# Kernel tuning notes

Hardware: AMD Instinct MI355X
Metric: run time of the kernel (lower is better)

The kernel has to match this reference:

```python
import jax, jax.numpy as jnp
import numpy as np

B, S, H = 4, 4096, 2048
NH, HD = 16, 128
DFF = 8192
CAPACITY = 0.5
EPS = 1e-5


def setup_inputs() -> dict:
    key = jax.random.key(0)
    ks = jax.random.split(key, 11)
    s_h = 1.0 / np.sqrt(H)
    s_f = 1.0 / np.sqrt(DFF)
    return {
        "hidden_states": jax.random.normal(ks[0], (B, S, H), jnp.float32),
        "w_router": jax.random.normal(ks[1], (H,), jnp.float32) * s_h,
        "b_router": jnp.zeros((1,), jnp.float32),
        "Wq": jax.random.normal(ks[2], (H, H), jnp.float32) * s_h,
        "Wk": jax.random.normal(ks[3], (H, H), jnp.float32) * s_h,
        "Wv": jax.random.normal(ks[4], (H, H), jnp.float32) * s_h,
        "Wo": jax.random.normal(ks[5], (H, H), jnp.float32) * s_h,
        "w_gate": jax.random.normal(ks[6], (H, DFF), jnp.float32) * s_h,
        "w_up": jax.random.normal(ks[7], (H, DFF), jnp.float32) * s_h,
        "w_down": jax.random.normal(ks[8], (DFF, H), jnp.float32) * s_f,
        "norm1_w": jnp.ones((H,), jnp.float32),
        "norm2_w": jnp.ones((H,), jnp.float32),
    }


def _rmsnorm(x, w):
    var = jnp.mean(jnp.square(x), axis=-1, keepdims=True)
    return x * jax.lax.rsqrt(var + EPS) * w


def reference(hidden_states, w_router, b_router, Wq, Wk, Wv, Wo,
              w_gate, w_up, w_down, norm1_w, norm2_w):
    x = hidden_states  # [B,S,H]
    # --- router: sigmoid(Wx+b), select top-k per row, ties via >= threshold ---
    logits = jnp.einsum("bsh,h->bs", x, w_router) + b_router[0]
    weights = jax.nn.sigmoid(logits)  # [B,S]
    k = max(1, int(CAPACITY * S))
    topk_vals, _ = jax.lax.top_k(weights, k)
    threshold = topk_vals[:, -1:]
    mask = weights >= threshold  # [B,S] bool

    # --- full block, computed per-token (attention is over seq_len==1) ---
    n1 = _rmsnorm(x, norm1_w)
    q = (n1 @ Wq).reshape(B, S, NH, HD)
    kk = (n1 @ Wk).reshape(B, S, NH, HD)
    v = (n1 @ Wv).reshape(B, S, NH, HD)
    # each selected token is its own length-1 sequence -> softmax over 1 pos == 1
    scores = jnp.einsum("bshd,bshd->bsh", q, kk) / np.sqrt(HD)
    attn_w = jax.nn.softmax(scores[..., None], axis=-1)  # [B,S,NH,1], all ones
    ctx = (attn_w * v).reshape(B, S, H)
    attn_out = ctx @ Wo

    res = x + attn_out
    n2 = _rmsnorm(res, norm2_w)
    ffn = (jax.nn.silu(n2 @ w_gate) * (n2 @ w_up)) @ w_down
    out_full = res + ffn

    # scatter back: non-selected tokens pass through unchanged
    out = jnp.where(mask[..., None], out_full, x)
    return out
```

## Files before the change

### kernel.cpp

```cpp
#include <hip/hip_runtime.h>
#include <cstdint>
#include <cstddef>

#define B_    4
#define S_    4096
#define H_    2048
#define DFF_  8192
#define KSEL  2048
#define CAP   2304
#define NTILE_PB 18
#define TCAP  (B_*CAP)
#define NRT   (TCAP/128)

typedef unsigned short ushort_t;
typedef __attribute__((ext_vector_type(8))) __bf16 bf16x8;
typedef __attribute__((ext_vector_type(4))) float f32x4;

__device__ __forceinline__ ushort_t f2bf(float f) {
  union { float f; uint32_t u; } v; v.f = f;
  uint32_t u = v.u;
  return (ushort_t)((u + 0x7FFFu + ((u >> 16) & 1u)) >> 16);
}

__device__ __forceinline__ void gload16(const void* g, void* l) {
  __builtin_amdgcn_global_load_lds(
      (const __attribute__((address_space(1))) void*)g,
      (__attribute__((address_space(3))) void*)l, 16, 0, 0);
}

__global__ __launch_bounds__(256) void wconvT_k(const float* __restrict__ W,
                                                ushort_t* __restrict__ Wt,
                                                int K, int N) {
  __shared__ float tile[64][65];
  int k0 = blockIdx.x * 64, n0 = blockIdx.y * 64;
  int tx = threadIdx.x & 63, ty = threadIdx.x >> 6;
  #pragma unroll
  for (int yy = ty; yy < 64; yy += 4)
    tile[yy][tx] = W[(size_t)(k0 + yy) * N + n0 + tx];
  __syncthreads();
  #pragma unroll
  for (int yy = ty; yy < 64; yy += 4)
    Wt[(size_t)(n0 + yy) * K + k0 + tx] = f2bf(tile[tx][yy]);
}

__global__ __launch_bounds__(256) void router_k(const float* __restrict__ x,
                                                const float* __restrict__ wr,
                                                const float* __restrict__ br,
                                                float* __restrict__ wts) {
  int t = blockIdx.x * 4 + (threadIdx.x >> 6);
  int lane = threadIdx.x & 63;
  const float4* xr = (const float4*)(x + (size_t)t * H_);
  const float4* w4 = (const float4*)wr;
  float s = 0.f;
  #pragma unroll
  for (int j = 0; j < 8; ++j) {
    float4 a = xr[lane + 64 * j], b = w4[lane + 64 * j];
    s = fmaf(a.x, b.x, s); s = fmaf(a.y, b.y, s);
    s = fmaf(a.z, b.z, s); s = fmaf(a.w, b.w, s);
  }
  #pragma unroll
  for (int o = 32; o > 0; o >>= 1) s += __shfl_xor(s, o, 64);
  if (lane == 0) wts[t] = 1.f / (1.f + expf(-(s + br[0])));
}

__global__ __launch_bounds__(1024) void kth_k(const float* __restrict__ wts,
                                              float* __restrict__ thr) {
  __shared__ float a[S_];
  int b = blockIdx.x, tid = threadIdx.x;
  const float* wb = wts + b * S_;
  for (int i = tid; i < S_; i += 1024) a[i] = wb[i];
  for (int size = 2; size <= S_; size <<= 1) {
    for (int stride = size >> 1; stride > 0; stride >>= 1) {
      __syncthreads();
      for (int t = tid; t < S_ / 2; t += 1024) {
        int i = ((t / stride) * (stride << 1)) + (t % stride);
        int j = i + stride;
        bool up = ((i & size) == 0);
        float ai = a[i], aj = a[j];
        if ((ai > aj) == up) { a[i] = aj; a[j] = ai; }
      }
    }
  }
  __syncthreads();
  if (tid == 0) thr[b] = a[S_ - KSEL];
}

__global__ __launch_bounds__(1024) void compact_k(const float* __restrict__ wts,
                                                  const float* __restrict__ thr,
                                                  int* __restrict__ idx,
                                                  int* __restrict__ counts) {
  __shared__ int sc[1024];
  int b = blockIdx.x, tid = threadIdx.x;
  float th = thr[b];
  int m[4], cnt = 0;
  #pragma unroll
  for (int e = 0; e < 4; ++e) {
    m[e] = (wts[b * S_ + tid * 4 + e] >= th) ? 1 : 0;
    cnt += m[e];
  }
  sc[tid] = cnt;
  __syncthreads();
  for (int off = 1; off < 1024; off <<= 1) {
    int add = (tid >= off) ? sc[tid - off] : 0;
    __syncthreads();
    sc[tid] += add;
    __syncthreads();
  }
  int excl = sc[tid] - cnt;
  int total = sc[1023];
  int cl = total < CAP ? total : CAP;
  #pragma unroll
  for (int e = 0; e < 4; ++e) {
    if (m[e]) {
      if (excl < CAP) idx[b * CAP + excl] = b * S_ + tid * 4 + e;
      excl++;
    }
  }
  for (int j2 = tid; j2 < CAP; j2 += 1024)
    if (j2 >= cl) idx[b * CAP + j2] = -1;
  if (tid == 0) counts[b] = cl;
}

template <int MODE>
__global__ __launch_bounds__(256) void rms_k(const float* __restrict__ src,
                                             const float* __restrict__ w,
                                             const int* __restrict__ idx,
                                             const int* __restrict__ counts,
                                             ushort_t* __restrict__ dst) {
  int r = blockIdx.x * 4 + (threadIdx.x >> 6);
  int lane = threadIdx.x & 63;
  ushort4* drow = (ushort4*)(dst + (size_t)r * H_);
  const float* s;
  if (MODE == 0) {
    int b = r / CAP, local = r % CAP;
    if (local >= counts[b]) {
      ushort4 z; z.x = z.y = z.z = z.w = 0;
      #pragma unroll
      for (int j = 0; j < 8; ++j) drow[lane + 64 * j] = z;
      return;
    }
    s = src + (size_t)idx[r] * H_;
  } else {
    s = src + (size_t)r * H_;
  }
  const float4* s4 = (const float4*)s;
  float4 v[8];
  float ss = 0.f;
  #pragma unroll
  for (int j = 0; j < 8; ++j) {
    v[j] = s4[lane + 64 * j];
    ss = fmaf(v[j].x, v[j].x, ss); ss = fmaf(v[j].y, v[j].y, ss);
    ss = fmaf(v[j].z, v[j].z, ss); ss = fmaf(v[j].w, v[j].w, ss);
  }
  #pragma unroll
  for (int o = 32; o > 0; o >>= 1) ss += __shfl_xor(ss, o, 64);
  float rstd = rsqrtf(ss * (1.f / H_) + 1e-5f);
  const float4* w4 = (const float4*)w;
  #pragma unroll
  for (int j = 0; j < 8; ++j) {
    float4 ww = w4[lane + 64 * j];
    ushort4 o4;
    o4.x = f2bf(v[j].x * rstd * ww.x);
    o4.y = f2bf(v[j].y * rstd * ww.y);
    o4.z = f2bf(v[j].z * rstd * ww.z);
    o4.w = f2bf(v[j].w * rstd * ww.w);
    drow[lane + 64 * j] = o4;
  }
}

__global__ void copy_k(const float4* __restrict__ in, float4* __restrict__ out,
                       int n) {
  int i = blockIdx.x * blockDim.x + threadIdx.x;
  int stride = gridDim.x * blockDim.x;
  for (; i < n; i += stride) out[i] = in[i];
}

template <int EPI>
__global__ __launch_bounds__(256) void gemm_k(const ushort_t* __restrict__ A,
                                              const ushort_t* __restrict__ Bt,
                                              int K, int N,
                                              const int* __restrict__ counts,
                                              const int* __restrict__ idx,
                                              const float* __restrict__ xres,
                                              float* __restrict__ outf,
                                              ushort_t* __restrict__ outh) {
  const int nt = N >> 7;
  const int rt = (int)blockIdx.x / nt;
  const int ct = (int)blockIdx.x % nt;
  const int bb = rt / NTILE_PB;
  const int local0 = (rt % NTILE_PB) << 7;
  if (local0 >= counts[bb]) return;

  __shared__ __align__(16) char lds[32768];
  char* ldsA = lds;
  char* ldsB = lds + 16384;

  const int tid = threadIdx.x;
  const int lane = tid & 63;
  const int wave = tid >> 6;
  const int wm = wave >> 1, wn = wave & 1;

  const int srow = tid >> 3;
  const int c16l = (tid & 7) ^ (srow & 7);
  const size_t Kb = (size_t)K * 2;
  const char* aSrc = (const char*)A + (size_t)(rt * 128 + srow) * Kb + (size_t)c16l * 16;
  const char* bSrc = (const char*)Bt + (size_t)(ct * 128 + srow) * Kb + (size_t)c16l * 16;
  char* aDst = ldsA + wave * 1024;
  char* bDst = ldsB + wave * 1024;

  const int frow = lane & 15;
  const int fk = lane >> 4;
  const int ax = frow & 7;

  f32x4 acc[4][4];
  #pragma unroll
  for (int i = 0; i < 4; ++i)
    #pragma unroll
    for (int j = 0; j < 4; ++j) acc[i][j] = (f32x4){0.f, 0.f, 0.f, 0.f};

  const int nkt = K >> 6;
  for (int kt = 0; kt < nkt; ++kt) {
    __syncthreads();
    #pragma unroll
    for (int inst = 0; inst < 4; ++inst) {
      gload16(aSrc + (size_t)inst * 32 * Kb + (size_t)kt * 128, aDst + inst * 4096);
      gload16(bSrc + (size_t)inst * 32 * Kb + (size_t)kt * 128, bDst + inst * 4096);
    }
    __syncthreads();
    #pragma unroll
    for (int ks = 0; ks < 2; ++ks) {
      bf16x8 af[4], bfv[4];
      #pragma unroll
      for (int i = 0; i < 4; ++i) {
        int ar = wm * 64 + i * 16 + frow;
        af[i] = *(const bf16x8*)(ldsA + ar * 128 + (((ks * 4 + fk) ^ ax) << 4));
        int br2 = wn * 64 + i * 16 + frow;
        bfv[i] = *(const bf16x8*)(ldsB + br2 * 128 + (((ks * 4 + fk) ^ ax) << 4));
      }
      #pragma unroll
      for (int i = 0; i < 4; ++i)
        #pragma unroll
        for (int j = 0; j < 4; ++j)
          acc[i][j] = __builtin_amdgcn_mfma_f32_16x16x32_bf16(af[i], bfv[j],
                                                              acc[i][j], 0, 0, 0);
    }
  }

  const int erow0 = rt * 128 + wm * 64;
  const int ecol0 = ct * 128 + wn * 64;
  const int rq = (lane >> 4) << 2;
  const int cc = lane & 15;
  #pragma unroll
  for (int i = 0; i < 4; ++i) {
    #pragma unroll
    for (int q = 0; q < 4; ++q) {
      int r = erow0 + i * 16 + rq + q;
      if (EPI == 0) {
        #pragma unroll
        for (int j = 0; j < 4; ++j)
          outh[(size_t)r * N + ecol0 + j * 16 + cc] = f2bf(acc[i][j][q]);
      } else if (EPI == 1) {
        int t = idx[r];
        #pragma unroll
        for (int j = 0; j < 4; ++j) {
          int c = ecol0 + j * 16 + cc;
          float xv = (t >= 0) ? xres[(size_t)t * H_ + c] : 0.f;
          outf[(size_t)r * H_ + c] = xv + acc[i][j][q];
        }
      } else {
        int t = idx[r];
        if (t >= 0) {
          #pragma unroll
          for (int j = 0; j < 4; ++j) {
            int c = ecol0 + j * 16 + cc;
            outf[(size_t)t * H_ + c] = xres[(size_t)r * H_ + c] + acc[i][j][q];
          }
        }
      }
    }
  }
}

__global__ __launch_bounds__(256) void gemm_dual_k(const ushort_t* __restrict__ A,
                                                   const ushort_t* __restrict__ Bg,
                                                   const ushort_t* __restrict__ Bu,
                                                   const int* __restrict__ counts,
                                                   ushort_t* __restrict__ Hb) {
  const int nt = DFF_ >> 7;
  const int rt = (int)blockIdx.x / nt;
  const int ct = (int)blockIdx.x % nt;
  const int bb = rt / NTILE_PB;
  const int local0 = (rt % NTILE_PB) << 7;
  if (local0 >= counts[bb]) return;

  __shared__ __align__(16) char lds[49152];
  char* ldsA = lds;
  char* ldsG = lds + 16384;
  char* ldsU = lds + 32768;

  const int tid = threadIdx.x;
  const int lane = tid & 63;
  const int wave = tid >> 6;
  const int wm = wave >> 1, wn = wave & 1;

  const int srow = tid >> 3;
  const int c16l = (tid & 7) ^ (srow & 7);
  const size_t Kb = (size_t)H_ * 2;
  const char* aSrc = (const char*)A + (size_t)(rt * 128 + srow) * Kb + (size_t)c16l * 16;
  const char* gSrc = (const char*)Bg + (size_t)(ct * 128 + srow) * Kb + (size_t)c16l * 16;
  const char* uSrc = (const char*)Bu + (size_t)(ct * 128 + srow) * Kb + (size_t)c16l * 16;
  char* aDst = ldsA + wave * 1024;
  char* gDst = ldsG + wave * 1024;
  char* uDst = ldsU + wave * 1024;

  const int frow = lane & 15;
  const int fk = lane >> 4;
  const int ax = frow & 7;

  f32x4 ag[4][4], au[4][4];
  #pragma unroll
  for (int i = 0; i < 4; ++i)
    #pragma unroll
    for (int j = 0; j < 4; ++j) {
      ag[i][j] = (f32x4){0.f, 0.f, 0.f, 0.f};
      au[i][j] = (f32x4){0.f, 0.f, 0.f, 0.f};
    }

  const int nkt = H_ >> 6;
  for (int kt = 0; kt < nkt; ++kt) {
    __syncthreads();
    #pragma unroll
    for (int inst = 0; inst < 4; ++inst) {
      gload16(aSrc + (size_t)inst * 32 * Kb + (size_t)kt * 128, aDst + inst * 4096);
      gload16(gSrc + (size_t)inst * 32 * Kb + (size_t)kt * 128, gDst + inst * 4096);
      gload16(uSrc + (size_t)inst * 32 * Kb + (size_t)kt * 128, uDst + inst * 4096);
    }
    __syncthreads();
    #pragma unroll
    for (int ks = 0; ks < 2; ++ks) {
      bf16x8 af[4], bg[4], bu[4];
      #pragma unroll
      for (int i = 0; i < 4; ++i) {
        int ar = wm * 64 + i * 16 + frow;
        int br2 = wn * 64 + i * 16 + frow;
        int co = (((ks * 4 + fk) ^ ax) << 4);
        af[i] = *(const bf16x8*)(ldsA + ar * 128 + co);
        bg[i] = *(const bf16x8*)(ldsG + br2 * 128 + co);
        bu[i] = *(const bf16x8*)(ldsU + br2 * 128 + co);
      }
      #pragma unroll
      for (int i = 0; i < 4; ++i)
        #pragma unroll
        for (int j = 0; j < 4; ++j) {
          ag[i][j] = __builtin_amdgcn_mfma_f32_16x16x32_bf16(af[i], bg[j], ag[i][j], 0, 0, 0);
          au[i][j] = __builtin_amdgcn_mfma_f32_16x16x32_bf16(af[i], bu[j], au[i][j], 0, 0, 0);
        }
    }
  }

  const int erow0 = rt * 128 + wm * 64;
  const int ecol0 = ct * 128 + wn * 64;
  const int rq = (lane >> 4) << 2;
  const int cc = lane & 15;
  #pragma unroll
  for (int i = 0; i < 4; ++i)
    #pragma unroll
    for (int q = 0; q < 4; ++q) {
      int r = erow0 + i * 16 + rq + q;
      #pragma unroll
      for (int j = 0; j < 4; ++j) {
        float g = ag[i][j][q], u = au[i][j][q];
        float h = (g / (1.f + expf(-g))) * u;
        Hb[(size_t)r * DFF_ + ecol0 + j * 16 + cc] = f2bf(h);
      }
    }
}

extern "C" void kernel_launch(void* const* d_in, const int* in_sizes, int n_in,
                              void* d_out, int out_size, void* d_ws, size_t ws_size,
                              hipStream_t stream) {
  const float* x   = (const float*)d_in[0];
  const float* wr  = (const float*)d_in[1];
  const float* br  = (const float*)d_in[2];
  const float* Wv  = (const float*)d_in[5];
  const float* Wo  = (const float*)d_in[6];
  const float* Wg  = (const float*)d_in[7];
  const float* Wu  = (const float*)d_in[8];
  const float* Wd  = (const float*)d_in[9];
  const float* n1w = (const float*)d_in[10];
  const float* n2w = (const float*)d_in[11];
  float* out = (float*)d_out;

  char* p = (char*)d_ws;
  auto alloc = [&](size_t bytes) {
    char* r = p;
    p += (bytes + 255) & ~(size_t)255;
    return r;
  };
  ushort_t* WvT = (ushort_t*)alloc((size_t)H_ * H_ * 2);
  ushort_t* WoT = (ushort_t*)alloc((size_t)H_ * H_ * 2);
  ushort_t* WgT = (ushort_t*)alloc((size_t)DFF_ * H_ * 2);
  ushort_t* WuT = (ushort_t*)alloc((size_t)DFF_ * H_ * 2);
  ushort_t* WdT = (ushort_t*)alloc((size_t)H_ * DFF_ * 2);
  float* wts    = (float*)alloc((size_t)B_ * S_ * 4);
  float* thr    = (float*)alloc(256);
  int* counts   = (int*)alloc(256);
  int* idx      = (int*)alloc((size_t)TCAP * 4);
  ushort_t* Xn1 = (ushort_t*)alloc((size_t)TCAP * H_ * 2);
  ushort_t* Vc  = (ushort_t*)alloc((size_t)TCAP * H_ * 2);
  float* RES    = (float*)alloc((size_t)TCAP * H_ * 4);
  ushort_t* Hb  = (ushort_t*)alloc((size_t)TCAP * DFF_ * 2);
  (void)ws_size; (void)in_sizes; (void)n_in; (void)out_size;

  wconvT_k<<<dim3(H_ / 64, H_ / 64), 256, 0, stream>>>(Wv, WvT, H_, H_);
  wconvT_k<<<dim3(H_ / 64, H_ / 64), 256, 0, stream>>>(Wo, WoT, H_, H_);
  wconvT_k<<<dim3(H_ / 64, DFF_ / 64), 256, 0, stream>>>(Wg, WgT, H_, DFF_);
  wconvT_k<<<dim3(H_ / 64, DFF_ / 64), 256, 0, stream>>>(Wu, WuT, H_, DFF_);
  wconvT_k<<<dim3(DFF_ / 64, H_ / 64), 256, 0, stream>>>(Wd, WdT, DFF_, H_);

  router_k<<<(B_ * S_) / 4, 256, 0, stream>>>(x, wr, br, wts);
  kth_k<<<B_, 1024, 0, stream>>>(wts, thr);
  compact_k<<<B_, 1024, 0, stream>>>(wts, thr, idx, counts);

  rms_k<0><<<TCAP / 4, 256, 0, stream>>>(x, n1w, idx, counts, Xn1);

  copy_k<<<2048, 256, 0, stream>>>((const float4*)x, (float4*)out,
                                   (B_ * S_ * H_) / 4);

  gemm_k<0><<<NRT * (H_ / 128), 256, 0, stream>>>(Xn1, WvT, H_, H_, counts, idx,
                                                  nullptr, nullptr, Vc);
  gemm_k<1><<<NRT * (H_ / 128), 256, 0, stream>>>(Vc, WoT, H_, H_, counts, idx,
                                                  x, RES, nullptr);
  rms_k<1><<<TCAP / 4, 256, 0, stream>>>(RES, n2w, idx, counts, Xn1);

  gemm_dual_k<<<NRT * (DFF_ / 128), 256, 0, stream>>>(Xn1, WgT, WuT, counts, Hb);

  gemm_k<2><<<NRT * (H_ / 128), 256, 0, stream>>>(Hb, WdT, DFF_, H_, counts, idx,
                                                  RES, out, nullptr);
}
```

Before: 2.126 ms.

## Replace GEMMs with 256x256 double-buffered 8-wave kernel and split gate/up

Replaces the 128x128 single-buffered GEMM kernels with one 256x256-tile, 512-thread kernel. It uses 128KB of dynamic LDS with double buffering so global-to-LDS prefetch of the next K tile overlaps the MFMA work, and it remaps block IDs in an XCD-aware way. The fused gate/up dual GEMM is split into two passes: the first writes the gate result as bf16, and the second reads it back to apply SiLU times up. This aims for more reuse per tile and hidden load latency, at the cost of extra traffic for the gate intermediate and coarser padding granularity for the per-batch token tiles.

```diff
diff --git a/kernel.cpp b/kernel.cpp
--- a/kernel.cpp
+++ b/kernel.cpp
@@ -8,9 +8,9 @@
 #define DFF_  8192
 #define KSEL  2048
 #define CAP   2304
-#define NTILE_PB 18
+#define TPB   9
 #define TCAP  (B_*CAP)
-#define NRT   (TCAP/128)
+#define NRT   (TCAP/256)
 
 typedef unsigned short ushort_t;
 typedef __attribute__((ext_vector_type(8))) __bf16 bf16x8;
@@ -21,12 +21,23 @@
   uint32_t u = v.u;
   return (ushort_t)((u + 0x7FFFu + ((u >> 16) & 1u)) >> 16);
 }
+__device__ __forceinline__ float bf2f(ushort_t h) {
+  union { uint32_t u; float f; } v; v.u = ((uint32_t)h) << 16;
+  return v.f;
+}
 
 __device__ __forceinline__ void gload16(const void* g, void* l) {
   __builtin_amdgcn_global_load_lds(
       (const __attribute__((address_space(1))) void*)g,
       (__attribute__((address_space(3))) void*)l, 16, 0, 0);
 }
+
+#define SBAR()                                  \
+  do {                                          \
+    asm volatile("" ::: "memory");              \
+    __builtin_amdgcn_s_barrier();               \
+    asm volatile("" ::: "memory");              \
+  } while (0)
 
 __global__ __launch_bounds__(256) void wconvT_k(const float* __restrict__ W,
                                                 ushort_t* __restrict__ Wt,
@@ -176,204 +187,158 @@
 }
 
 template <int EPI>
-__global__ __launch_bounds__(256) void gemm_k(const ushort_t* __restrict__ A,
-                                              const ushort_t* __restrict__ Bt,
-                                              int K, int N,
-                                              const int* __restrict__ counts,
-                                              const int* __restrict__ idx,
-                                              const float* __restrict__ xres,
-                                              float* __restrict__ outf,
-                                              ushort_t* __restrict__ outh) {
-  const int nt = N >> 7;
-  const int rt = (int)blockIdx.x / nt;
-  const int ct = (int)blockIdx.x % nt;
-  const int bb = rt / NTILE_PB;
-  const int local0 = (rt % NTILE_PB) << 7;
+__global__ __launch_bounds__(512, 2) void gemm8_k(
+    const ushort_t* __restrict__ A,
+    const ushort_t* __restrict__ Bt,
+    int K, int N, int nct,
+    const int* __restrict__ counts,
+    const int* __restrict__ idx,
+    const float* __restrict__ xres,
+    const ushort_t* __restrict__ gsrc,
+    float* __restrict__ outf,
+    ushort_t* __restrict__ outh) {
+  const int nwg = (int)gridDim.x;
+  const int bid = (int)blockIdx.x;
+  const int cpx = nwg >> 3;
+  const int wg = (bid & 7) * cpx + (bid >> 3);
+  const int rt = wg / nct;
+  const int ct = wg % nct;
+  const int bb = rt / TPB;
+  const int local0 = (rt % TPB) << 8;
   if (local0 >= counts[bb]) return;
 
-  __shared__ __align__(16) char lds[32768];
-  char* ldsA = lds;
-  char* ldsB = lds + 16384;
-
-  const int tid = threadIdx.x;
+  extern __shared__ __align__(16) char lds[];
+
+  const int tid = (int)threadIdx.x;
   const int lane = tid & 63;
   const int wave = tid >> 6;
-  const int wm = wave >> 1, wn = wave & 1;
+  const int wm = wave >> 2;
+  const int wn = wave & 3;
 
   const int srow = tid >> 3;
-  const int c16l = (tid & 7) ^ (srow & 7);
+  const int schunk = (tid & 7) ^ (srow & 7);
   const size_t Kb = (size_t)K * 2;
-  const char* aSrc = (const char*)A + (size_t)(rt * 128 + srow) * Kb + (size_t)c16l * 16;
-  const char* bSrc = (const char*)Bt + (size_t)(ct * 128 + srow) * Kb + (size_t)c16l * 16;
-  char* aDst = ldsA + wave * 1024;
-  char* bDst = ldsB + wave * 1024;
+  const char* aS = (const char*)A + (size_t)(rt * 256 + srow) * Kb + (size_t)schunk * 16;
+  const char* bS = (const char*)Bt + (size_t)(ct * 256 + srow) * Kb + (size_t)schunk * 16;
 
   const int frow = lane & 15;
   const int fk = lane >> 4;
-  const int ax = frow & 7;
-
-  f32x4 acc[4][4];
+
+  f32x4 acc[8][4];
+  #pragma unroll
+  for (int m = 0; m < 8; ++m)
+    #pragma unroll
+    for (int n = 0; n < 4; ++n) acc[m][n] = (f32x4){0.f, 0.f, 0.f, 0.f};
+
   #pragma unroll
   for (int i = 0; i < 4; ++i)
-    #pragma unroll
-    for (int j = 0; j < 4; ++j) acc[i][j] = (f32x4){0.f, 0.f, 0.f, 0.f};
+    gload16(aS + (size_t)i * 64 * Kb, lds + i * 8192 + wave * 1024);
+  #pragma unroll
+  for (int i = 0; i < 4; ++i)
+    gload16(bS + (size_t)i * 64 * Kb, lds + 65536 + i * 8192 + wave * 1024);
+  asm volatile("s_waitcnt vmcnt(0)" ::: "memory");
+  SBAR();
 
   const int nkt = K >> 6;
   for (int kt = 0; kt < nkt; ++kt) {
-    __syncthreads();
+    const int po = (kt & 1) << 15;
+    const int no = po ^ 32768;
+    const char* curA = lds + po;
+    const char* curB = lds + 65536 + po;
+    char* nxtA = lds + no;
+    char* nxtB = lds + 65536 + no;
+    const bool pre = (kt + 1 < nkt);
+    const size_t kcol = (size_t)(kt + 1) * 128;
+    bf16x8 bfr[4][2];
+
     #pragma unroll
-    for (int inst = 0; inst < 4; ++inst) {
-      gload16(aSrc + (size_t)inst * 32 * Kb + (size_t)kt * 128, aDst + inst * 4096);
-      gload16(bSrc + (size_t)inst * 32 * Kb + (size_t)kt * 128, bDst + inst * 4096);
+    for (int q = 0; q < 4; ++q) {
+      if (q == 0 && pre) {
+        #pragma unroll
+        for (int i = 0; i < 4; ++i)
+          gload16(aS + (size_t)i * 64 * Kb + kcol, nxtA + i * 8192 + wave * 1024);
+      }
+      if (q == 1 && pre) {
+        #pragma unroll
+        for (int i = 0; i < 4; ++i)
+          gload16(bS + (size_t)i * 64 * Kb + kcol, nxtB + i * 8192 + wave * 1024);
+      }
+      bf16x8 af[2][2];
+      #pragma unroll
+      for (int i = 0; i < 2; ++i) {
+        const int row = wm * 128 + (2 * q + i) * 16 + frow;
+        #pragma unroll
+        for (int ks = 0; ks < 2; ++ks)
+          af[i][ks] = *(const bf16x8*)(curA + row * 128 +
+                                       (((ks * 4 + fk) ^ (row & 7)) << 4));
+      }
+      if (q == 0) {
+        #pragma unroll
+        for (int n = 0; n < 4; ++n) {
+          const int row = wn * 64 + n * 16 + frow;
+          #pragma unroll
+          for (int ks = 0; ks < 2; ++ks)
+            bfr[n][ks] = *(const bf16x8*)(curB + row * 128 +
+                                          (((ks * 4 + fk) ^ (row & 7)) << 4));
+        }
+      }
+      SBAR();
+      __builtin_amdgcn_s_setprio(1);
+      #pragma unroll
+      for (int i = 0; i < 2; ++i)
+        #pragma unroll
+        for (int ks = 0; ks < 2; ++ks)
+          #pragma unroll
+          for (int n = 0; n < 4; ++n)
+            acc[2 * q + i][n] = __builtin_amdgcn_mfma_f32_16x16x32_bf16(
+                af[i][ks], bfr[n][ks], acc[2 * q + i][n], 0, 0, 0);
+      __builtin_amdgcn_s_setprio(0);
+      if (q == 3) asm volatile("s_waitcnt vmcnt(0)" ::: "memory");
+      SBAR();
     }
-    __syncthreads();
-    #pragma unroll
-    for (int ks = 0; ks < 2; ++ks) {
-      bf16x8 af[4], bfv[4];
-      #pragma unroll
-      for (int i = 0; i < 4; ++i) {
-        int ar = wm * 64 + i * 16 + frow;
-        af[i] = *(const bf16x8*)(ldsA + ar * 128 + (((ks * 4 + fk) ^ ax) << 4));
-        int br2 = wn * 64 + i * 16 + frow;
-        bfv[i] = *(const bf16x8*)(ldsB + br2 * 128 + (((ks * 4 + fk) ^ ax) << 4));
-      }
-      #pragma unroll
-      for (int i = 0; i < 4; ++i)
-        #pragma unroll
-        for (int j = 0; j < 4; ++j)
-          acc[i][j] = __builtin_amdgcn_mfma_f32_16x16x32_bf16(af[i], bfv[j],
-                                                              acc[i][j], 0, 0, 0);
-    }
-  }
-
-  const int erow0 = rt * 128 + wm * 64;
-  const int ecol0 = ct * 128 + wn * 64;
+  }
+
+  const int erow0 = rt * 256 + wm * 128;
+  const int ecol0 = ct * 256 + wn * 64;
   const int rq = (lane >> 4) << 2;
   const int cc = lane & 15;
   #pragma unroll
-  for (int i = 0; i < 4; ++i) {
+  for (int m = 0; m < 8; ++m) {
     #pragma unroll
-    for (int q = 0; q < 4; ++q) {
-      int r = erow0 + i * 16 + rq + q;
+    for (int qq = 0; qq < 4; ++qq) {
+      const int r = erow0 + m * 16 + rq + qq;
       if (EPI == 0) {
         #pragma unroll
-        for (int j = 0; j < 4; ++j)
-          outh[(size_t)r * N + ecol0 + j * 16 + cc] = f2bf(acc[i][j][q]);
+        for (int n = 0; n < 4; ++n)
+          outh[(size_t)r * N + ecol0 + n * 16 + cc] = f2bf(acc[m][n][qq]);
       } else if (EPI == 1) {
-        int t = idx[r];
-        #pragma unroll
-        for (int j = 0; j < 4; ++j) {
-          int c = ecol0 + j * 16 + cc;
-          float xv = (t >= 0) ? xres[(size_t)t * H_ + c] : 0.f;
-          outf[(size_t)r * H_ + c] = xv + acc[i][j][q];
+        const int t = idx[r];
+        #pragma unroll
+        for (int n = 0; n < 4; ++n) {
+          const int c = ecol0 + n * 16 + cc;
+          const float xv = (t >= 0) ? xres[(size_t)t * H_ + c] : 0.f;
+          outf[(size_t)r * H_ + c] = xv + acc[m][n][qq];
+        }
+      } else if (EPI == 2) {
+        #pragma unroll
+        for (int n = 0; n < 4; ++n) {
+          const size_t o = (size_t)r * N + ecol0 + n * 16 + cc;
+          const float g = bf2f(gsrc[o]);
+          const float h = (g / (1.f + expf(-g))) * acc[m][n][qq];
+          outh[o] = f2bf(h);
         }
       } else {
-        int t = idx[r];
+        const int t = idx[r];
         if (t >= 0) {
           #pragma unroll
-          for (int j = 0; j < 4; ++j) {
-            int c = ecol0 + j * 16 + cc;
-            outf[(size_t)t * H_ + c] = xres[(size_t)r * H_ + c] + acc[i][j][q];
+          for (int n = 0; n < 4; ++n) {
+            const int c = ecol0 + n * 16 + cc;
+            outf[(size_t)t * H_ + c] = xres[(size_t)r * H_ + c] + acc[m][n][qq];
           }
         }
       }
     }
   }
-}
-
-__global__ __launch_bounds__(256) void gemm_dual_k(const ushort_t* __restrict__ A,
-                                                   const ushort_t* __restrict__ Bg,
-                                                   const ushort_t* __restrict__ Bu,
-                                                   const int* __restrict__ counts,
-                                                   ushort_t* __restrict__ Hb) {
-  const int nt = DFF_ >> 7;
-  const int rt = (int)blockIdx.x / nt;
-  const int ct = (int)blockIdx.x % nt;
-  const int bb = rt / NTILE_PB;
-  const int local0 = (rt % NTILE_PB) << 7;
-  if (local0 >= counts[bb]) return;
-
-  __shared__ __align__(16) char lds[49152];
-  char* ldsA = lds;
-  char* ldsG = lds + 16384;
-  char* ldsU = lds + 32768;
-
-  const int tid = threadIdx.x;
-  const int lane = tid & 63;
-  const int wave = tid >> 6;
-  const int wm = wave >> 1, wn = wave & 1;
-
-  const int srow = tid >> 3;
-  const int c16l = (tid & 7) ^ (srow & 7);
-  const size_t Kb = (size_t)H_ * 2;
-  const char* aSrc = (const char*)A + (size_t)(rt * 128 + srow) * Kb + (size_t)c16l * 16;
-  const char* gSrc = (const char*)Bg + (size_t)(ct * 128 + srow) * Kb + (size_t)c16l * 16;
-  const char* uSrc = (const char*)Bu + (size_t)(ct * 128 + srow) * Kb + (size_t)c16l * 16;
-  char* aDst = ldsA + wave * 1024;
-  char* gDst = ldsG + wave * 1024;
-  char* uDst = ldsU + wave * 1024;
-
-  const int frow = lane & 15;
-  const int fk = lane >> 4;
-  const int ax = frow & 7;
-
-  f32x4 ag[4][4], au[4][4];
-  #pragma unroll
-  for (int i = 0; i < 4; ++i)
-    #pragma unroll
-    for (int j = 0; j < 4; ++j) {
-      ag[i][j] = (f32x4){0.f, 0.f, 0.f, 0.f};
-      au[i][j] = (f32x4){0.f, 0.f, 0.f, 0.f};
-    }
-
-  const int nkt = H_ >> 6;
-  for (int kt = 0; kt < nkt; ++kt) {
-    __syncthreads();
-    #pragma unroll
-    for (int inst = 0; inst < 4; ++inst) {
-      gload16(aSrc + (size_t)inst * 32 * Kb + (size_t)kt * 128, aDst + inst * 4096);
-      gload16(gSrc + (size_t)inst * 32 * Kb + (size_t)kt * 128, gDst + inst * 4096);
-      gload16(uSrc + (size_t)inst * 32 * Kb + (size_t)kt * 128, uDst + inst * 4096);
-    }
-    __syncthreads();
-    #pragma unroll
-    for (int ks = 0; ks < 2; ++ks) {
-      bf16x8 af[4], bg[4], bu[4];
-      #pragma unroll
-      for (int i = 0; i < 4; ++i) {
-        int ar = wm * 64 + i * 16 + frow;
-        int br2 = wn * 64 + i * 16 + frow;
-        int co = (((ks * 4 + fk) ^ ax) << 4);
-        af[i] = *(const bf16x8*)(ldsA + ar * 128 + co);
-        bg[i] = *(const bf16x8*)(ldsG + br2 * 128 + co);
-        bu[i] = *(const bf16x8*)(ldsU + br2 * 128 + co);
-      }
-      #pragma unroll
-      for (int i = 0; i < 4; ++i)
-        #pragma unroll
-        for (int j = 0; j < 4; ++j) {
-          ag[i][j] = __builtin_amdgcn_mfma_f32_16x16x32_bf16(af[i], bg[j], ag[i][j], 0, 0, 0);
-          au[i][j] = __builtin_amdgcn_mfma_f32_16x16x32_bf16(af[i], bu[j], au[i][j], 0, 0, 0);
-        }
-    }
-  }
-
-  const int erow0 = rt * 128 + wm * 64;
-  const int ecol0 = ct * 128 + wn * 64;
-  const int rq = (lane >> 4) << 2;
-  const int cc = lane & 15;
-  #pragma unroll
-  for (int i = 0; i < 4; ++i)
-    #pragma unroll
-    for (int q = 0; q < 4; ++q) {
-      int r = erow0 + i * 16 + rq + q;
-      #pragma unroll
-      for (int j = 0; j < 4; ++j) {
-        float g = ag[i][j][q], u = au[i][j][q];
-        float h = (g / (1.f + expf(-g))) * u;
-        Hb[(size_t)r * DFF_ + ecol0 + j * 16 + cc] = f2bf(h);
-      }
-    }
 }
 
 extern "C" void kernel_launch(void* const* d_in, const int* in_sizes, int n_in,
@@ -427,14 +392,16 @@
   copy_k<<<2048, 256, 0, stream>>>((const float4*)x, (float4*)out,
                                    (B_ * S_ * H_) / 4);
 
-  gemm_k<0><<<NRT * (H_ / 128), 256, 0, stream>>>(Xn1, WvT, H_, H_, counts, idx,
-                                                  nullptr, nullptr, Vc);
-  gemm_k<1><<<NRT * (H_ / 128), 256, 0, stream>>>(Vc, WoT, H_, H_, counts, idx,
-                                                  x, RES, nullptr);
+  const size_t LDSB = 131072;
+  gemm8_k<0><<<NRT * (H_ / 256), 512, LDSB, stream>>>(
+      Xn1, WvT, H_, H_, H_ / 256, counts, idx, nullptr, nullptr, nullptr, Vc);
+  gemm8_k<1><<<NRT * (H_ / 256), 512, LDSB, stream>>>(
+      Vc, WoT, H_, H_, H_ / 256, counts, idx, x, nullptr, RES, nullptr);
   rms_k<1><<<TCAP / 4, 256, 0, stream>>>(RES, n2w, idx, counts, Xn1);
-
-  gemm_dual_k<<<NRT * (DFF_ / 128), 256, 0, stream>>>(Xn1, WgT, WuT, counts, Hb);
-
-  gemm_k<2><<<NRT * (H_ / 128), 256, 0, stream>>>(Hb, WdT, DFF_, H_, counts, idx,
-                                                  RES, out, nullptr);
-}
+  gemm8_k<0><<<NRT * (DFF_ / 256), 512, LDSB, stream>>>(
+      Xn1, WgT, H_, DFF_, DFF_ / 256, counts, idx, nullptr, nullptr, nullptr, Hb);
+  gemm8_k<2><<<NRT * (DFF_ / 256), 512, LDSB, stream>>>(
+      Xn1, WuT, H_, DFF_, DFF_ / 256, counts, idx, nullptr, Hb, nullptr, Hb);
+  gemm8_k<3><<<NRT * (H_ / 256), 512, LDSB, stream>>>(
+      Hb, WdT, DFF_, H_, H_ / 256, counts, idx, RES, nullptr, out, nullptr);
+}
```

Result: faster. 1.963 ms (-7.7%).

## Split dual gate/up GEMM into two single GEMMs and swizzle workgroups across XCDs

Applied to the files above, without the earlier changes.

Replaces the fused gate/up GEMM, which used 48KB of LDS and two accumulator sets, with two passes of the generic single-B GEMM. The gate pass writes bf16 gate values into Hb, and the up pass reads them back and applies SiLU times up in its epilogue. It also remaps block indices so that consecutive tiles spread across the 8 XCDs, aiming for better L2 locality. The split lowers register and LDS pressure, which should raise occupancy, but it reads the A operand twice, adds a bf16 round trip of the gate values through memory, and rounds gate to bf16 before the SiLU.

```diff
diff --git a/kernel.cpp b/kernel.cpp
--- a/kernel.cpp
+++ b/kernel.cpp
@@ -8,7 +8,7 @@
 #define DFF_  8192
 #define KSEL  2048
 #define CAP   2304
-#define NTILE_PB 18
+#define TPB   18
 #define TCAP  (B_*CAP)
 #define NRT   (TCAP/128)
 
@@ -20,6 +20,10 @@
   union { float f; uint32_t u; } v; v.f = f;
   uint32_t u = v.u;
   return (ushort_t)((u + 0x7FFFu + ((u >> 16) & 1u)) >> 16);
+}
+__device__ __forceinline__ float bf2f(ushort_t h) {
+  union { uint32_t u; float f; } v; v.u = ((uint32_t)h) << 16;
+  return v.f;
 }
 
 __device__ __forceinline__ void gload16(const void* g, void* l) {
@@ -178,24 +182,27 @@
 template <int EPI>
 __global__ __launch_bounds__(256) void gemm_k(const ushort_t* __restrict__ A,
                                               const ushort_t* __restrict__ Bt,
-                                              int K, int N,
+                                              int K, int N, int nct,
                                               const int* __restrict__ counts,
                                               const int* __restrict__ idx,
                                               const float* __restrict__ xres,
                                               float* __restrict__ outf,
                                               ushort_t* __restrict__ outh) {
-  const int nt = N >> 7;
-  const int rt = (int)blockIdx.x / nt;
-  const int ct = (int)blockIdx.x % nt;
-  const int bb = rt / NTILE_PB;
-  const int local0 = (rt % NTILE_PB) << 7;
+  const int nwg = (int)gridDim.x;
+  const int bid = (int)blockIdx.x;
+  const int cpx = nwg >> 3;
+  const int wg = (bid & 7) * cpx + (bid >> 3);
+  const int rt = wg / nct;
+  const int ct = wg % nct;
+  const int bb = rt / TPB;
+  const int local0 = (rt % TPB) << 7;
   if (local0 >= counts[bb]) return;
 
   __shared__ __align__(16) char lds[32768];
   char* ldsA = lds;
   char* ldsB = lds + 16384;
 
-  const int tid = threadIdx.x;
+  const int tid = (int)threadIdx.x;
   const int lane = tid & 63;
   const int wave = tid >> 6;
   const int wm = wave >> 1, wn = wave & 1;
@@ -267,6 +274,13 @@
           float xv = (t >= 0) ? xres[(size_t)t * H_ + c] : 0.f;
           outf[(size_t)r * H_ + c] = xv + acc[i][j][q];
         }
+      } else if (EPI == 2) {
+        #pragma unroll
+        for (int j = 0; j < 4; ++j) {
+          size_t o = (size_t)r * N + ecol0 + j * 16 + cc;
+          float g = bf2f(outh[o]);
+          outh[o] = f2bf((g / (1.f + expf(-g))) * acc[i][j][q]);
+        }
       } else {
         int t = idx[r];
         if (t >= 0) {
@@ -279,101 +293,6 @@
       }
     }
   }
-}
-
-__global__ __launch_bounds__(256) void gemm_dual_k(const ushort_t* __restrict__ A,
-                                                   const ushort_t* __restrict__ Bg,
-                                                   const ushort_t* __restrict__ Bu,
-                                                   const int* __restrict__ counts,
-                                                   ushort_t* __restrict__ Hb) {
-  const int nt = DFF_ >> 7;
-  const int rt = (int)blockIdx.x / nt;
-  const int ct = (int)blockIdx.x % nt;
-  const int bb = rt / NTILE_PB;
-  const int local0 = (rt % NTILE_PB) << 7;
-  if (local0 >= counts[bb]) return;
-
-  __shared__ __align__(16) char lds[49152];
-  char* ldsA = lds;
-  char* ldsG = lds + 16384;
-  char* ldsU = lds + 32768;
-
-  const int tid = threadIdx.x;
-  const int lane = tid & 63;
-  const int wave = tid >> 6;
-  const int wm = wave >> 1, wn = wave & 1;
-
-  const int srow = tid >> 3;
-  const int c16l = (tid & 7) ^ (srow & 7);
-  const size_t Kb = (size_t)H_ * 2;
-  const char* aSrc = (const char*)A + (size_t)(rt * 128 + srow) * Kb + (size_t)c16l * 16;
-  const char* gSrc = (const char*)Bg + (size_t)(ct * 128 + srow) * Kb + (size_t)c16l * 16;
-  const char* uSrc = (const char*)Bu + (size_t)(ct * 128 + srow) * Kb + (size_t)c16l * 16;
-  char* aDst = ldsA + wave * 1024;
-  char* gDst = ldsG + wave * 1024;
-  char* uDst = ldsU + wave * 1024;
-
-  const int frow = lane & 15;
-  const int fk = lane >> 4;
-  const int ax = frow & 7;
-
-  f32x4 ag[4][4], au[4][4];
-  #pragma unroll
-  for (int i = 0; i < 4; ++i)
-    #pragma unroll
-    for (int j = 0; j < 4; ++j) {
-      ag[i][j] = (f32x4){0.f, 0.f, 0.f, 0.f};
-      au[i][j] = (f32x4){0.f, 0.f, 0.f, 0.f};
-    }
-
-  const int nkt = H_ >> 6;
-  for (int kt = 0; kt < nkt; ++kt) {
-    __syncthreads();
-    #pragma unroll
-    for (int inst = 0; inst < 4; ++inst) {
-      gload16(aSrc + (size_t)inst * 32 * Kb + (size_t)kt * 128, aDst + inst * 4096);
-      gload16(gSrc + (size_t)inst * 32 * Kb + (size_t)kt * 128, gDst + inst * 4096);
-      gload16(uSrc + (size_t)inst * 32 * Kb + (size_t)kt * 128, uDst + inst * 4096);
-    }
-    __syncthreads();
-    #pragma unroll
-    for (int ks = 0; ks < 2; ++ks) {
-      bf16x8 af[4], bg[4], bu[4];
-      #pragma unroll
-      for (int i = 0; i < 4; ++i) {
-        int ar = wm * 64 + i * 16 + frow;
-        int br2 = wn * 64 + i * 16 + frow;
-        int co = (((ks * 4 + fk) ^ ax) << 4);
-        af[i] = *(const bf16x8*)(ldsA + ar * 128 + co);
-        bg[i] = *(const bf16x8*)(ldsG + br2 * 128 + co);
-        bu[i] = *(const bf16x8*)(ldsU + br2 * 128 + co);
-      }
-      #pragma unroll
-      for (int i = 0; i < 4; ++i)
-        #pragma unroll
-        for (int j = 0; j < 4; ++j) {
-          ag[i][j] = __builtin_amdgcn_mfma_f32_16x16x32_bf16(af[i], bg[j], ag[i][j], 0, 0, 0);
-          au[i][j] = __builtin_amdgcn_mfma_f32_16x16x32_bf16(af[i], bu[j], au[i][j], 0, 0, 0);
-        }
-    }
-  }
-
-  const int erow0 = rt * 128 + wm * 64;
-  const int ecol0 = ct * 128 + wn * 64;
-  const int rq = (lane >> 4) << 2;
-  const int cc = lane & 15;
-  #pragma unroll
-  for (int i = 0; i < 4; ++i)
-    #pragma unroll
-    for (int q = 0; q < 4; ++q) {
-      int r = erow0 + i * 16 + rq + q;
-      #pragma unroll
-      for (int j = 0; j < 4; ++j) {
-        float g = ag[i][j][q], u = au[i][j][q];
-        float h = (g / (1.f + expf(-g))) * u;
-        Hb[(size_t)r * DFF_ + ecol0 + j * 16 + cc] = f2bf(h);
-      }
-    }
 }
 
 extern "C" void kernel_launch(void* const* d_in, const int* in_sizes, int n_in,
@@ -427,14 +346,15 @@
   copy_k<<<2048, 256, 0, stream>>>((const float4*)x, (float4*)out,
                                    (B_ * S_ * H_) / 4);
 
-  gemm_k<0><<<NRT * (H_ / 128), 256, 0, stream>>>(Xn1, WvT, H_, H_, counts, idx,
-                                                  nullptr, nullptr, Vc);
-  gemm_k<1><<<NRT * (H_ / 128), 256, 0, stream>>>(Vc, WoT, H_, H_, counts, idx,
-                                                  x, RES, nullptr);
+  gemm_k<0><<<NRT * (H_ / 128), 256, 0, stream>>>(
+      Xn1, WvT, H_, H_, H_ / 128, counts, idx, nullptr, nullptr, Vc);
+  gemm_k<1><<<NRT * (H_ / 128), 256, 0, stream>>>(
+      Vc, WoT, H_, H_, H_ / 128, counts, idx, x, RES, nullptr);
   rms_k<1><<<TCAP / 4, 256, 0, stream>>>(RES, n2w, idx, counts, Xn1);
-
-  gemm_dual_k<<<NRT * (DFF_ / 128), 256, 0, stream>>>(Xn1, WgT, WuT, counts, Hb);
-
-  gemm_k<2><<<NRT * (H_ / 128), 256, 0, stream>>>(Hb, WdT, DFF_, H_, counts, idx,
-                                                  RES, out, nullptr);
-}
+  gemm_k<0><<<NRT * (DFF_ / 128), 256, 0, stream>>>(
+      Xn1, WgT, H_, DFF_, DFF_ / 128, counts, idx, nullptr, nullptr, Hb);
+  gemm_k<2><<<NRT * (DFF_ / 128), 256, 0, stream>>>(
+      Xn1, WuT, H_, DFF_, DFF_ / 128, counts, idx, nullptr, nullptr, Hb);
+  gemm_k<3><<<NRT * (H_ / 128), 256, 0, stream>>>(
+      Hb, WdT, DFF_, H_, H_ / 128, counts, idx, RES, out, nullptr);
+}
```

After: 1.996 ms. 6.1% less time.
